# Kernel optimization log

Measured on AMD Instinct MI355X. Metric: run time of the kernel, lower is better.

Reference implementation:

```python
import jax, jax.numpy as jnp
import numpy as np

D = 2048        # hidden_size
F = 2048        # intermediate_size
E = 8           # num_local_experts
TOPK = 2        # num_experts_per_tok
ALPHA = 1.702   # gpt-oss swiglu alpha
LIMIT = 7.0     # gpt-oss clamp limit
AUX_COEF = 0.01


def setup_inputs() -> dict:
    key = jax.random.key(0)
    ks = jax.random.split(key, 7)
    s = 0.02
    return {
        "x": jax.random.normal(ks[0], (4, 1024, D), dtype=jnp.float32),
        "router_w": jax.random.normal(ks[1], (D, E), dtype=jnp.float32) * s,
        "router_b": jnp.zeros((E,), dtype=jnp.float32),
        "w_gate_up": jax.random.normal(ks[2], (E, D, 2 * F), dtype=jnp.float32) * s,
        "b_gate_up": jnp.zeros((E, 2 * F), dtype=jnp.float32),
        "w_down": jax.random.normal(ks[3], (E, F, D), dtype=jnp.float32) * s,
        "b_down": jnp.zeros((E, D), dtype=jnp.float32),
    }


def _moe(x, router_w, router_b, w_gate_up, b_gate_up, w_down, b_down):
    B, S, _ = x.shape
    xt = x.reshape(B * S, D)                                   # [T, D]
    T = xt.shape[0]

    # --- router ---
    logits = xt @ router_w + router_b                          # [T, E]
    full_probs = jax.nn.softmax(logits, axis=-1)               # [T, E]
    top_logits, top_idx = jax.lax.top_k(logits, TOPK)          # [T, k]
    routing_weights = jax.nn.softmax(top_logits, axis=-1)      # [T, k] (gpt-oss: softmax over top-k only)

    onehot = jax.nn.one_hot(top_idx, E, dtype=xt.dtype)        # [T, k, E]
    combine_w = jnp.einsum("tk,tke->te", routing_weights, onehot)  # [T, E]

    # --- experts (dense reference over all experts, masked combine) ---
    gu = jnp.einsum("td,edh->eth", xt, w_gate_up) + b_gate_up[:, None, :]  # [E, T, 2F]
    gate = gu[..., 0::2]                                       # interleaved gate
    up = gu[..., 1::2]                                         # interleaved up
    gate = jnp.minimum(gate, LIMIT)
    up = jnp.clip(up, -LIMIT, LIMIT)
    glu = gate * jax.nn.sigmoid(gate * ALPHA)
    act = (up + 1.0) * glu                                     # [E, T, F]
    expert_out = jnp.einsum("etf,efd->etd", act, w_down) + b_down[:, None, :]  # [E, T, D]

    out = jnp.einsum("etd,te->td", expert_out, combine_w).reshape(B, S, D)

    # --- routing stats / aux loss (Switch/Mixtral-style) ---
    dispatch_frac = jnp.mean(jnp.sum(onehot, axis=1), axis=0) / TOPK   # [E], sums to 1
    mean_probs = jnp.mean(full_probs, axis=0)                          # [E]
    expert_loads = dispatch_frac
    load_balancing_loss = AUX_COEF * E * jnp.sum(dispatch_frac * mean_probs)
    return out, expert_loads, load_balancing_loss


def reference(x, router_w, router_b, w_gate_up, b_gate_up, w_down, b_down):
    return _moe(x, router_w, router_b, w_gate_up, b_gate_up, w_down, b_down)
```

## Files before the change

kernel.cpp:

```cpp
#include <hip/hip_runtime.h>
#include <hip/hip_bf16.h>

#define TD 2048
#define TF 2048
#define NE 8
#define NT 4096
#define NTOPK 2

typedef __attribute__((ext_vector_type(4))) float f32x4;
typedef __attribute__((ext_vector_type(8))) short bf16x8;
typedef __attribute__((ext_vector_type(4))) short s16x4;

#define WS_XBF   ((size_t)0)
#define WS_ACT   ((size_t)16 << 20)
#define WS_WGU   ((size_t)48 << 20)
#define WS_WD    ((size_t)176 << 20)
#define WS_PROBS ((size_t)240 << 20)
#define WS_TOK   (WS_PROBS + (size_t)NT * NE * 4)
#define WS_WT    (WS_TOK + (size_t)NE * NT * 4)
#define WS_CNT   (WS_WT + (size_t)NE * NT * 4)
#define WS_OFF   (WS_CNT + 64)

__device__ __forceinline__ unsigned short f2bf(float f) {
  union { float f; unsigned u; } v; v.f = f;
  unsigned r = v.u + 0x7FFFu + ((v.u >> 16) & 1u);
  return (unsigned short)(r >> 16);
}

__device__ __forceinline__ void gload_lds16(const void* g, void* l) {
  __builtin_amdgcn_global_load_lds(
      (const __attribute__((address_space(1))) void*)g,
      (__attribute__((address_space(3))) void*)l, 16, 0, 0);
}

__global__ void k_cvt_x(const float* __restrict__ x, unsigned short* __restrict__ xbf) {
  int i = blockIdx.x * 256 + threadIdx.x;
  float4 v = ((const float4*)x)[i];
  s16x4 r;
  r[0] = (short)f2bf(v.x); r[1] = (short)f2bf(v.y);
  r[2] = (short)f2bf(v.z); r[3] = (short)f2bf(v.w);
  ((s16x4*)xbf)[i] = r;
}

__global__ void k_router(const float* __restrict__ x, const float* __restrict__ rw,
                         const float* __restrict__ rb, float* __restrict__ probs,
                         int* __restrict__ tok, float* __restrict__ wt,
                         int* __restrict__ counts) {
  const int t = blockIdx.x;
  const int l = threadIdx.x;
  const float* xr = x + (size_t)t * TD;
  float a0 = 0, a1 = 0, a2 = 0, a3 = 0, a4 = 0, a5 = 0, a6 = 0, a7 = 0;
#pragma unroll 4
  for (int j = 0; j < TD / 64; j++) {
    int d = j * 64 + l;
    float xv = xr[d];
    const float4* wp = (const float4*)(rw + (size_t)d * NE);
    float4 w0 = wp[0], w1 = wp[1];
    a0 += xv * w0.x; a1 += xv * w0.y; a2 += xv * w0.z; a3 += xv * w0.w;
    a4 += xv * w1.x; a5 += xv * w1.y; a6 += xv * w1.z; a7 += xv * w1.w;
  }
#pragma unroll
  for (int off = 32; off > 0; off >>= 1) {
    a0 += __shfl_xor(a0, off); a1 += __shfl_xor(a1, off);
    a2 += __shfl_xor(a2, off); a3 += __shfl_xor(a3, off);
    a4 += __shfl_xor(a4, off); a5 += __shfl_xor(a5, off);
    a6 += __shfl_xor(a6, off); a7 += __shfl_xor(a7, off);
  }
  if (l == 0) {
    float lg[NE] = { a0 + rb[0], a1 + rb[1], a2 + rb[2], a3 + rb[3],
                     a4 + rb[4], a5 + rb[5], a6 + rb[6], a7 + rb[7] };
    float mx = lg[0];
#pragma unroll
    for (int e = 1; e < NE; e++) mx = fmaxf(mx, lg[e]);
    float pe[NE]; float s = 0.f;
#pragma unroll
    for (int e = 0; e < NE; e++) { pe[e] = __expf(lg[e] - mx); s += pe[e]; }
    float inv = 1.f / s;
#pragma unroll
    for (int e = 0; e < NE; e++) probs[(size_t)t * NE + e] = pe[e] * inv;
    int i0 = 0; float b0 = lg[0];
#pragma unroll
    for (int e = 1; e < NE; e++) if (lg[e] > b0) { b0 = lg[e]; i0 = e; }
    int i1 = (i0 == 0) ? 1 : 0; float b1 = lg[i1];
#pragma unroll
    for (int e = 0; e < NE; e++)
      if (e != i0 && lg[e] > b1) { b1 = lg[e]; i1 = e; }
    float e1 = __expf(b1 - b0);
    float rs = 1.f / (1.f + e1);
    float w0v = rs;
    float w1v = e1 * rs;
    int p0 = atomicAdd(&counts[i0], 1);
    tok[i0 * NT + p0] = t; wt[i0 * NT + p0] = w0v;
    int p1 = atomicAdd(&counts[i1], 1);
    tok[i1 * NT + p1] = t; wt[i1 * NT + p1] = w1v;
  }
}

__global__ void k_finalize(const float* __restrict__ probs, const int* __restrict__ counts,
                           int* __restrict__ offsets, float* __restrict__ tail) {
  __shared__ float sh[4 * NE];
  int tid = threadIdx.x;
  float s[NE] = {0, 0, 0, 0, 0, 0, 0, 0};
  for (int t = tid; t < NT; t += 256) {
#pragma unroll
    for (int e = 0; e < NE; e++) s[e] += probs[(size_t)t * NE + e];
  }
#pragma unroll
  for (int off = 32; off > 0; off >>= 1) {
#pragma unroll
    for (int e = 0; e < NE; e++) s[e] += __shfl_xor(s[e], off);
  }
  if ((tid & 63) == 0) {
#pragma unroll
    for (int e = 0; e < NE; e++) sh[(tid >> 6) * NE + e] = s[e];
  }
  __syncthreads();
  if (tid == 0) {
    float loss = 0.f; int off = 0;
#pragma unroll
    for (int e = 0; e < NE; e++) {
      float mp = (sh[e] + sh[NE + e] + sh[2 * NE + e] + sh[3 * NE + e]) * (1.f / NT);
      int c = counts[e];
      offsets[e] = off; off += c;
      float df = (float)c / (float)(NT * NTOPK);
      tail[e] = df;
      loss += df * mp;
    }
    tail[NE] = 0.01f * (float)NE * loss;
  }
}

template <int REMAP>
__global__ void k_transpose(const float* __restrict__ W, unsigned short* __restrict__ Wt,
                            int R , int C ) {
  __shared__ unsigned short tile[64][72];
  const int e = blockIdx.z;
  const float* We = W + (size_t)e * R * C;
  unsigned short* Ot = Wt + (size_t)e * R * C;
  const int k0 = blockIdx.y * 64, c0 = blockIdx.x * 64;
  const int tid = threadIdx.x;
  {
    const int lr = tid >> 2, lq = tid & 3;
    const float* src = We + (size_t)(k0 + lr) * C + c0 + lq * 16;
#pragma unroll
    for (int q = 0; q < 4; q++) {
      float4 v = *(const float4*)(src + q * 4);
      int c = lq * 16 + q * 4;
      tile[lr][c + 0] = f2bf(v.x); tile[lr][c + 1] = f2bf(v.y);
      tile[lr][c + 2] = f2bf(v.z); tile[lr][c + 3] = f2bf(v.w);
    }
  }
  __syncthreads();
  {
    const int oc = tid >> 2, kq = tid & 3;
    const int n_src = c0 + oc;
    const int orow = REMAP ? ((n_src >> 1) + (n_src & 1) * TF) : n_src;
    unsigned short* dst = Ot + (size_t)orow * R + k0 + kq * 16;
#pragma unroll
    for (int g = 0; g < 4; g++) {
      s16x4 v;
#pragma unroll
      for (int i = 0; i < 4; i++) v[i] = (short)tile[kq * 16 + g * 4 + i][oc];
      *(s16x4*)(dst + g * 4) = v;
    }
  }
}

__global__ __launch_bounds__(256) void k_gemm1(
    const unsigned short* __restrict__ xbf, const int* __restrict__ tok,
    const int* __restrict__ counts, const int* __restrict__ offsets,
    const unsigned short* __restrict__ wgu, const float* __restrict__ bgu,
    unsigned short* __restrict__ act) {
  const int e = blockIdx.z;
  const int cnt = counts[e];
  const int m0 = blockIdx.y * 128;
  if (m0 >= cnt) return;
  const int n0 = blockIdx.x * 64;
  const int offe = offsets[e];
  const unsigned short* Bg = wgu + (size_t)e * (2 * TF) * TD;
  __shared__ unsigned short lA[128 * 32];
  __shared__ unsigned short lB[128 * 32];
  const int tid = threadIdx.x, wid = tid >> 6, lane = tid & 63;

  const unsigned short* srcA[2];
  const unsigned short* srcB[2];
#pragma unroll
  for (int j = 0; j < 2; j++) {
    int idx = j * 256 + tid, r = idx >> 2, q = idx & 3;
    int rr = min(m0 + r, cnt - 1);
    srcA[j] = xbf + (size_t)tok[e * NT + rr] * TD + q * 8;
    int srow = (r < 64) ? (n0 + r) : (TF + n0 + (r - 64));
    srcB[j] = Bg + (size_t)srow * TD + q * 8;
  }
  const int kc = (lane >> 4) * 8, cA = lane & 15;
  int aoff[2], boff[8];
#pragma unroll
  for (int mr = 0; mr < 2; mr++) aoff[mr] = (wid * 32 + mr * 16 + cA) * 32 + kc;
#pragma unroll
  for (int nf = 0; nf < 8; nf++) boff[nf] = (nf * 16 + cA) * 32 + kc;

  f32x4 acc[2][8] = {};

  for (int kt = 0; kt < TD / 32; kt++) {
    const int k0 = kt * 32;
    __syncthreads();
    gload_lds16(srcA[0] + k0, &lA[(size_t)tid * 8]);
    gload_lds16(srcA[1] + k0, &lA[(size_t)(256 + tid) * 8]);
    gload_lds16(srcB[0] + k0, &lB[(size_t)tid * 8]);
    gload_lds16(srcB[1] + k0, &lB[(size_t)(256 + tid) * 8]);
    __syncthreads();
    bf16x8 af0 = *(const bf16x8*)&lA[aoff[0]];
    bf16x8 af1 = *(const bf16x8*)&lA[aoff[1]];
#pragma unroll
    for (int nf = 0; nf < 8; nf++) {
      bf16x8 bfr = *(const bf16x8*)&lB[boff[nf]];
      acc[0][nf] = __builtin_amdgcn_mfma_f32_16x16x32_bf16(af0, bfr, acc[0][nf], 0, 0, 0);
      acc[1][nf] = __builtin_amdgcn_mfma_f32_16x16x32_bf16(af1, bfr, acc[1][nf], 0, 0, 0);
    }
  }

  const float* be = bgu + (size_t)e * 2 * TF;
#pragma unroll
  for (int nf = 0; nf < 4; nf++) {
    int col = n0 + nf * 16 + cA;
    float bgate = be[2 * col], bup = be[2 * col + 1];
#pragma unroll
    for (int mr = 0; mr < 2; mr++) {
#pragma unroll
      for (int r = 0; r < 4; r++) {
        int row = wid * 32 + mr * 16 + (lane >> 4) * 4 + r;
        if (m0 + row < cnt) {
          float g = acc[mr][nf][r] + bgate;
          float u = acc[mr][nf + 4][r] + bup;
          g = fminf(g, 7.0f);
          u = fminf(fmaxf(u, -7.0f), 7.0f);
          float glu = g * (1.0f / (1.0f + __expf(-1.702f * g)));
          float a = (u + 1.0f) * glu;
          act[(size_t)(offe + m0 + row) * TF + col] = f2bf(a);
        }
      }
    }
  }
}

__global__ __launch_bounds__(256) void k_gemm2(
    const unsigned short* __restrict__ act, const int* __restrict__ tok,
    const float* __restrict__ wt, const int* __restrict__ counts,
    const int* __restrict__ offsets, const unsigned short* __restrict__ wd,
    const float* __restrict__ bd, float* __restrict__ out) {
  const int e = blockIdx.z;
  const int cnt = counts[e];
  const int m0 = blockIdx.y * 128;
  if (m0 >= cnt) return;
  const int d0 = blockIdx.x * 128;
  const int offe = offsets[e];
  const unsigned short* Bd = wd + (size_t)e * TD * TF;
  __shared__ unsigned short lA[128 * 32];
  __shared__ unsigned short lB[128 * 32];
  const int tid = threadIdx.x, wid = tid >> 6, lane = tid & 63;

  const unsigned short* srcA[2];
  const unsigned short* srcB[2];
#pragma unroll
  for (int j = 0; j < 2; j++) {
    int idx = j * 256 + tid, r = idx >> 2, q = idx & 3;
    int rr = min(m0 + r, cnt - 1);
    srcA[j] = act + (size_t)(offe + rr) * TF + q * 8;
    srcB[j] = Bd + (size_t)(d0 + r) * TF + q * 8;
  }
  const int kc = (lane >> 4) * 8, cA = lane & 15;
  int aoff[2], boff[8];
#pragma unroll
  for (int mr = 0; mr < 2; mr++) aoff[mr] = (wid * 32 + mr * 16 + cA) * 32 + kc;
#pragma unroll
  for (int nf = 0; nf < 8; nf++) boff[nf] = (nf * 16 + cA) * 32 + kc;

  f32x4 acc[2][8] = {};

  for (int kt = 0; kt < TF / 32; kt++) {
    const int k0 = kt * 32;
    __syncthreads();
    gload_lds16(srcA[0] + k0, &lA[(size_t)tid * 8]);
    gload_lds16(srcA[1] + k0, &lA[(size_t)(256 + tid) * 8]);
    gload_lds16(srcB[0] + k0, &lB[(size_t)tid * 8]);
    gload_lds16(srcB[1] + k0, &lB[(size_t)(256 + tid) * 8]);
    __syncthreads();
    bf16x8 af0 = *(const bf16x8*)&lA[aoff[0]];
    bf16x8 af1 = *(const bf16x8*)&lA[aoff[1]];
#pragma unroll
    for (int nf = 0; nf < 8; nf++) {
      bf16x8 bfr = *(const bf16x8*)&lB[boff[nf]];
      acc[0][nf] = __builtin_amdgcn_mfma_f32_16x16x32_bf16(af0, bfr, acc[0][nf], 0, 0, 0);
      acc[1][nf] = __builtin_amdgcn_mfma_f32_16x16x32_bf16(af1, bfr, acc[1][nf], 0, 0, 0);
    }
  }

  const float* bde = bd + (size_t)e * TD;
#pragma unroll
  for (int nf = 0; nf < 8; nf++) {
    int col = d0 + nf * 16 + cA;
    float bc = bde[col];
#pragma unroll
    for (int mr = 0; mr < 2; mr++) {
#pragma unroll
      for (int r = 0; r < 4; r++) {
        int row = wid * 32 + mr * 16 + (lane >> 4) * 4 + r;
        int rowe = m0 + row;
        if (rowe < cnt) {
          float v = acc[mr][nf][r] + bc;
          int tk = tok[e * NT + rowe];
          float w = wt[e * NT + rowe];
          atomicAdd(&out[(size_t)tk * TD + col], w * v);
        }
      }
    }
  }
}

extern "C" void kernel_launch(void* const* d_in, const int* in_sizes, int n_in,
                              void* d_out, int out_size, void* d_ws, size_t ws_size,
                              hipStream_t stream) {
  const float* x   = (const float*)d_in[0];
  const float* rw  = (const float*)d_in[1];
  const float* rb  = (const float*)d_in[2];
  const float* wgu = (const float*)d_in[3];
  const float* bgu = (const float*)d_in[4];
  const float* wdn = (const float*)d_in[5];
  const float* bdn = (const float*)d_in[6];
  float* out = (float*)d_out;
  char* ws = (char*)d_ws;

  unsigned short* xbf  = (unsigned short*)(ws + WS_XBF);
  unsigned short* act  = (unsigned short*)(ws + WS_ACT);
  unsigned short* wgut = (unsigned short*)(ws + WS_WGU);
  unsigned short* wdt  = (unsigned short*)(ws + WS_WD);
  float* probs = (float*)(ws + WS_PROBS);
  int*   tokl  = (int*)(ws + WS_TOK);
  float* wtl   = (float*)(ws + WS_WT);
  int*   cnts  = (int*)(ws + WS_CNT);
  int*   offs  = (int*)(ws + WS_OFF);

  hipMemsetAsync(out, 0, (size_t)NT * TD * sizeof(float), stream);
  hipMemsetAsync(cnts, 0, NE * sizeof(int), stream);

  k_cvt_x<<<(NT * TD) / 1024, 256, 0, stream>>>(x, xbf);
  k_router<<<NT, 64, 0, stream>>>(x, rw, rb, probs, tokl, wtl, cnts);
  k_finalize<<<1, 256, 0, stream>>>(probs, cnts, offs, out + (size_t)NT * TD);
  k_transpose<1><<<dim3(4096 / 64, 2048 / 64, NE), 256, 0, stream>>>(wgu, wgut, TD, 2 * TF);
  k_transpose<0><<<dim3(2048 / 64, 2048 / 64, NE), 256, 0, stream>>>(wdn, wdt, TF, TD);
  k_gemm1<<<dim3(TF / 64, NT / 128, NE), 256, 0, stream>>>(xbf, tokl, cnts, offs, wgut, bgu, act);
  k_gemm2<<<dim3(TD / 128, NT / 128, NE), 256, 0, stream>>>(act, tokl, wtl, cnts, offs, wdt, bdn, out);
}
```

Measured before the change: 1.016 ms.

## Replace atomic scatter with gather combine, retile GEMM warps, widen transpose tiles

The router now records each token's two (expert, slot) pairs so the down-projection can write weighted rows into a contiguous per-slot buffer. A separate combine kernel then gathers and sums them, which removes the float atomics and the memset of the output. Both GEMMs switch from a 1x4 warp layout (2x8 fragments per warp) to a 2x2 layout (4x4 fragments) to improve fragment reuse from LDS. Grid axes are swapped so consecutive blocks share weight columns. The weight transpose uses larger 256-row tiles with XOR-swizzled LDS and 16-byte stores. In exchange it adds a 64 MB intermediate buffer write and read plus one extra launch.

```diff
diff --git a/kernel.cpp b/kernel.cpp
--- a/kernel.cpp
+++ b/kernel.cpp
@@ -14,11 +14,13 @@
 #define WS_XBF   ((size_t)0)
 #define WS_ACT   ((size_t)16 << 20)
 #define WS_WGU   ((size_t)48 << 20)
+#define WS_EO    ((size_t)48 << 20)
 #define WS_WD    ((size_t)176 << 20)
 #define WS_PROBS ((size_t)240 << 20)
 #define WS_TOK   (WS_PROBS + (size_t)NT * NE * 4)
 #define WS_WT    (WS_TOK + (size_t)NE * NT * 4)
-#define WS_CNT   (WS_WT + (size_t)NE * NT * 4)
+#define WS_INV   (WS_WT + (size_t)NE * NT * 4)
+#define WS_CNT   (WS_INV + (size_t)NT * 16)
 #define WS_OFF   (WS_CNT + 64)
 
 __device__ __forceinline__ unsigned short f2bf(float f) {
@@ -45,7 +47,7 @@
 __global__ void k_router(const float* __restrict__ x, const float* __restrict__ rw,
                          const float* __restrict__ rb, float* __restrict__ probs,
                          int* __restrict__ tok, float* __restrict__ wt,
-                         int* __restrict__ counts) {
+                         int4* __restrict__ inv, int* __restrict__ counts) {
   const int t = blockIdx.x;
   const int l = threadIdx.x;
   const float* xr = x + (size_t)t * TD;
@@ -75,9 +77,9 @@
     float pe[NE]; float s = 0.f;
 #pragma unroll
     for (int e = 0; e < NE; e++) { pe[e] = __expf(lg[e] - mx); s += pe[e]; }
-    float inv = 1.f / s;
-#pragma unroll
-    for (int e = 0; e < NE; e++) probs[(size_t)t * NE + e] = pe[e] * inv;
+    float inv_s = 1.f / s;
+#pragma unroll
+    for (int e = 0; e < NE; e++) probs[(size_t)t * NE + e] = pe[e] * inv_s;
     int i0 = 0; float b0 = lg[0];
 #pragma unroll
     for (int e = 1; e < NE; e++) if (lg[e] > b0) { b0 = lg[e]; i0 = e; }
@@ -93,6 +95,7 @@
     tok[i0 * NT + p0] = t; wt[i0 * NT + p0] = w0v;
     int p1 = atomicAdd(&counts[i1], 1);
     tok[i1 * NT + p1] = t; wt[i1 * NT + p1] = w1v;
+    inv[t] = make_int4(i0, p0, i1, p1);
   }
 }
 
@@ -131,37 +134,42 @@
 }
 
 template <int REMAP>
-__global__ void k_transpose(const float* __restrict__ W, unsigned short* __restrict__ Wt,
-                            int R , int C ) {
-  __shared__ unsigned short tile[64][72];
+__global__ __launch_bounds__(256) void k_transpose(
+    const float* __restrict__ W, unsigned short* __restrict__ Wt, int R, int C) {
+  __shared__ unsigned short lds[256 * 64];
   const int e = blockIdx.z;
   const float* We = W + (size_t)e * R * C;
   unsigned short* Ot = Wt + (size_t)e * R * C;
-  const int k0 = blockIdx.y * 64, c0 = blockIdx.x * 64;
+  const int k0 = blockIdx.y * 256, c0 = blockIdx.x * 64;
   const int tid = threadIdx.x;
   {
-    const int lr = tid >> 2, lq = tid & 3;
-    const float* src = We + (size_t)(k0 + lr) * C + c0 + lq * 16;
-#pragma unroll
-    for (int q = 0; q < 4; q++) {
-      float4 v = *(const float4*)(src + q * 4);
-      int c = lq * 16 + q * 4;
-      tile[lr][c + 0] = f2bf(v.x); tile[lr][c + 1] = f2bf(v.y);
-      tile[lr][c + 2] = f2bf(v.z); tile[lr][c + 3] = f2bf(v.w);
+    const int rsub = tid >> 4;
+    const int cq = tid & 15;
+#pragma unroll
+    for (int p = 0; p < 16; p++) {
+      int row = p * 16 + rsub;
+      float4 v = *(const float4*)(We + (size_t)(k0 + row) * C + c0 + cq * 4);
+      s16x4 b;
+      b[0] = f2bf(v.x); b[1] = f2bf(v.y); b[2] = f2bf(v.z); b[3] = f2bf(v.w);
+      *(s16x4*)&lds[row * 64 + ((cq ^ (row & 15)) << 2)] = b;
     }
   }
   __syncthreads();
   {
-    const int oc = tid >> 2, kq = tid & 3;
-    const int n_src = c0 + oc;
+    const int c = tid & 63, seg = tid >> 6;
+    const int n_src = c0 + c;
     const int orow = REMAP ? ((n_src >> 1) + (n_src & 1) * TF) : n_src;
-    unsigned short* dst = Ot + (size_t)orow * R + k0 + kq * 16;
-#pragma unroll
-    for (int g = 0; g < 4; g++) {
-      s16x4 v;
-#pragma unroll
-      for (int i = 0; i < 4; i++) v[i] = (short)tile[kq * 16 + g * 4 + i][oc];
-      *(s16x4*)(dst + g * 4) = v;
+    unsigned short* dst = Ot + (size_t)orow * R + k0 + seg * 64;
+    const int ccq = c >> 2, cr = c & 3;
+#pragma unroll
+    for (int g = 0; g < 8; g++) {
+      bf16x8 val;
+#pragma unroll
+      for (int ii = 0; ii < 8; ii++) {
+        int k = seg * 64 + g * 8 + ii;
+        val[ii] = (short)lds[k * 64 + (((ccq ^ (k & 15)) << 2) | cr)];
+      }
+      *(bf16x8*)(dst + g * 8) = val;
     }
   }
 }
@@ -173,14 +181,15 @@
     unsigned short* __restrict__ act) {
   const int e = blockIdx.z;
   const int cnt = counts[e];
-  const int m0 = blockIdx.y * 128;
+  const int m0 = blockIdx.x * 128;
   if (m0 >= cnt) return;
-  const int n0 = blockIdx.x * 64;
+  const int n0 = blockIdx.y * 64;
   const int offe = offsets[e];
   const unsigned short* Bg = wgu + (size_t)e * (2 * TF) * TD;
   __shared__ unsigned short lA[128 * 32];
   __shared__ unsigned short lB[128 * 32];
   const int tid = threadIdx.x, wid = tid >> 6, lane = tid & 63;
+  const int wr = wid >> 1, wc = wid & 1;
 
   const unsigned short* srcA[2];
   const unsigned short* srcB[2];
@@ -192,14 +201,17 @@
     int srow = (r < 64) ? (n0 + r) : (TF + n0 + (r - 64));
     srcB[j] = Bg + (size_t)srow * TD + q * 8;
   }
-  const int kc = (lane >> 4) * 8, cA = lane & 15;
-  int aoff[2], boff[8];
-#pragma unroll
-  for (int mr = 0; mr < 2; mr++) aoff[mr] = (wid * 32 + mr * 16 + cA) * 32 + kc;
-#pragma unroll
-  for (int nf = 0; nf < 8; nf++) boff[nf] = (nf * 16 + cA) * 32 + kc;
-
-  f32x4 acc[2][8] = {};
+  const int cA = lane & 15, q = lane >> 4, kc = q * 8;
+  int aoff[4], boff[4];
+#pragma unroll
+  for (int m = 0; m < 4; m++) aoff[m] = (wr * 64 + m * 16 + cA) * 32 + kc;
+#pragma unroll
+  for (int n = 0; n < 4; n++) {
+    int brow = (n < 2) ? (wc * 32 + n * 16) : (64 + wc * 32 + (n - 2) * 16);
+    boff[n] = (brow + cA) * 32 + kc;
+  }
+
+  f32x4 acc[4][4] = {};
 
   for (int kt = 0; kt < TD / 32; kt++) {
     const int k0 = kt * 32;
@@ -209,29 +221,31 @@
     gload_lds16(srcB[0] + k0, &lB[(size_t)tid * 8]);
     gload_lds16(srcB[1] + k0, &lB[(size_t)(256 + tid) * 8]);
     __syncthreads();
-    bf16x8 af0 = *(const bf16x8*)&lA[aoff[0]];
-    bf16x8 af1 = *(const bf16x8*)&lA[aoff[1]];
-#pragma unroll
-    for (int nf = 0; nf < 8; nf++) {
-      bf16x8 bfr = *(const bf16x8*)&lB[boff[nf]];
-      acc[0][nf] = __builtin_amdgcn_mfma_f32_16x16x32_bf16(af0, bfr, acc[0][nf], 0, 0, 0);
-      acc[1][nf] = __builtin_amdgcn_mfma_f32_16x16x32_bf16(af1, bfr, acc[1][nf], 0, 0, 0);
+    bf16x8 af[4];
+#pragma unroll
+    for (int m = 0; m < 4; m++) af[m] = *(const bf16x8*)&lA[aoff[m]];
+#pragma unroll
+    for (int n = 0; n < 4; n++) {
+      bf16x8 bfr = *(const bf16x8*)&lB[boff[n]];
+#pragma unroll
+      for (int m = 0; m < 4; m++)
+        acc[m][n] = __builtin_amdgcn_mfma_f32_16x16x32_bf16(af[m], bfr, acc[m][n], 0, 0, 0);
     }
   }
 
   const float* be = bgu + (size_t)e * 2 * TF;
 #pragma unroll
-  for (int nf = 0; nf < 4; nf++) {
-    int col = n0 + nf * 16 + cA;
-    float bgate = be[2 * col], bup = be[2 * col + 1];
-#pragma unroll
-    for (int mr = 0; mr < 2; mr++) {
+  for (int n = 0; n < 2; n++) {
+    int col = n0 + wc * 32 + n * 16 + cA;
+    float bg = be[2 * col], bu = be[2 * col + 1];
+#pragma unroll
+    for (int m = 0; m < 4; m++) {
 #pragma unroll
       for (int r = 0; r < 4; r++) {
-        int row = wid * 32 + mr * 16 + (lane >> 4) * 4 + r;
+        int row = wr * 64 + m * 16 + q * 4 + r;
         if (m0 + row < cnt) {
-          float g = acc[mr][nf][r] + bgate;
-          float u = acc[mr][nf + 4][r] + bup;
+          float g = acc[m][n][r] + bg;
+          float u = acc[m][n + 2][r] + bu;
           g = fminf(g, 7.0f);
           u = fminf(fmaxf(u, -7.0f), 7.0f);
           float glu = g * (1.0f / (1.0f + __expf(-1.702f * g)));
@@ -244,20 +258,21 @@
 }
 
 __global__ __launch_bounds__(256) void k_gemm2(
-    const unsigned short* __restrict__ act, const int* __restrict__ tok,
-    const float* __restrict__ wt, const int* __restrict__ counts,
-    const int* __restrict__ offsets, const unsigned short* __restrict__ wd,
-    const float* __restrict__ bd, float* __restrict__ out) {
+    const unsigned short* __restrict__ act, const float* __restrict__ wt,
+    const int* __restrict__ counts, const int* __restrict__ offsets,
+    const unsigned short* __restrict__ wd, const float* __restrict__ bd,
+    float* __restrict__ eo) {
   const int e = blockIdx.z;
   const int cnt = counts[e];
-  const int m0 = blockIdx.y * 128;
+  const int m0 = blockIdx.x * 128;
   if (m0 >= cnt) return;
-  const int d0 = blockIdx.x * 128;
+  const int d0 = blockIdx.y * 128;
   const int offe = offsets[e];
   const unsigned short* Bd = wd + (size_t)e * TD * TF;
   __shared__ unsigned short lA[128 * 32];
   __shared__ unsigned short lB[128 * 32];
   const int tid = threadIdx.x, wid = tid >> 6, lane = tid & 63;
+  const int wr = wid >> 1, wc = wid & 1;
 
   const unsigned short* srcA[2];
   const unsigned short* srcB[2];
@@ -268,14 +283,14 @@
     srcA[j] = act + (size_t)(offe + rr) * TF + q * 8;
     srcB[j] = Bd + (size_t)(d0 + r) * TF + q * 8;
   }
-  const int kc = (lane >> 4) * 8, cA = lane & 15;
-  int aoff[2], boff[8];
-#pragma unroll
-  for (int mr = 0; mr < 2; mr++) aoff[mr] = (wid * 32 + mr * 16 + cA) * 32 + kc;
-#pragma unroll
-  for (int nf = 0; nf < 8; nf++) boff[nf] = (nf * 16 + cA) * 32 + kc;
-
-  f32x4 acc[2][8] = {};
+  const int cA = lane & 15, q = lane >> 4, kc = q * 8;
+  int aoff[4], boff[4];
+#pragma unroll
+  for (int m = 0; m < 4; m++) aoff[m] = (wr * 64 + m * 16 + cA) * 32 + kc;
+#pragma unroll
+  for (int n = 0; n < 4; n++) boff[n] = (wc * 64 + n * 16 + cA) * 32 + kc;
+
+  f32x4 acc[4][4] = {};
 
   for (int kt = 0; kt < TF / 32; kt++) {
     const int k0 = kt * 32;
@@ -285,36 +300,49 @@
     gload_lds16(srcB[0] + k0, &lB[(size_t)tid * 8]);
     gload_lds16(srcB[1] + k0, &lB[(size_t)(256 + tid) * 8]);
     __syncthreads();
-    bf16x8 af0 = *(const bf16x8*)&lA[aoff[0]];
-    bf16x8 af1 = *(const bf16x8*)&lA[aoff[1]];
-#pragma unroll
-    for (int nf = 0; nf < 8; nf++) {
-      bf16x8 bfr = *(const bf16x8*)&lB[boff[nf]];
-      acc[0][nf] = __builtin_amdgcn_mfma_f32_16x16x32_bf16(af0, bfr, acc[0][nf], 0, 0, 0);
-      acc[1][nf] = __builtin_amdgcn_mfma_f32_16x16x32_bf16(af1, bfr, acc[1][nf], 0, 0, 0);
+    bf16x8 af[4];
+#pragma unroll
+    for (int m = 0; m < 4; m++) af[m] = *(const bf16x8*)&lA[aoff[m]];
+#pragma unroll
+    for (int n = 0; n < 4; n++) {
+      bf16x8 bfr = *(const bf16x8*)&lB[boff[n]];
+#pragma unroll
+      for (int m = 0; m < 4; m++)
+        acc[m][n] = __builtin_amdgcn_mfma_f32_16x16x32_bf16(af[m], bfr, acc[m][n], 0, 0, 0);
     }
   }
 
   const float* bde = bd + (size_t)e * TD;
 #pragma unroll
-  for (int nf = 0; nf < 8; nf++) {
-    int col = d0 + nf * 16 + cA;
+  for (int n = 0; n < 4; n++) {
+    int col = d0 + wc * 64 + n * 16 + cA;
     float bc = bde[col];
 #pragma unroll
-    for (int mr = 0; mr < 2; mr++) {
+    for (int m = 0; m < 4; m++) {
 #pragma unroll
       for (int r = 0; r < 4; r++) {
-        int row = wid * 32 + mr * 16 + (lane >> 4) * 4 + r;
+        int row = wr * 64 + m * 16 + q * 4 + r;
         int rowe = m0 + row;
         if (rowe < cnt) {
-          float v = acc[mr][nf][r] + bc;
-          int tk = tok[e * NT + rowe];
           float w = wt[e * NT + rowe];
-          atomicAdd(&out[(size_t)tk * TD + col], w * v);
+          eo[(size_t)(offe + rowe) * TD + col] = w * (acc[m][n][r] + bc);
         }
       }
     }
   }
+}
+
+__global__ void k_combine(const float* __restrict__ eo, const int4* __restrict__ inv,
+                          const int* __restrict__ offs, float* __restrict__ out) {
+  int i = blockIdx.x * 256 + threadIdx.x;
+  int t = i >> 9;
+  int c = i & 511;
+  int4 v = inv[t];
+  int s0 = offs[v.x] + v.y, s1 = offs[v.z] + v.w;
+  float4 a = ((const float4*)eo)[(size_t)s0 * 512 + c];
+  float4 b = ((const float4*)eo)[(size_t)s1 * 512 + c];
+  float4 r; r.x = a.x + b.x; r.y = a.y + b.y; r.z = a.z + b.z; r.w = a.w + b.w;
+  ((float4*)out)[i] = r;
 }
 
 extern "C" void kernel_launch(void* const* d_in, const int* in_sizes, int n_in,
@@ -334,20 +362,22 @@
   unsigned short* act  = (unsigned short*)(ws + WS_ACT);
   unsigned short* wgut = (unsigned short*)(ws + WS_WGU);
   unsigned short* wdt  = (unsigned short*)(ws + WS_WD);
+  float* eo    = (float*)(ws + WS_EO);
   float* probs = (float*)(ws + WS_PROBS);
   int*   tokl  = (int*)(ws + WS_TOK);
   float* wtl   = (float*)(ws + WS_WT);
+  int4*  invm  = (int4*)(ws + WS_INV);
   int*   cnts  = (int*)(ws + WS_CNT);
   int*   offs  = (int*)(ws + WS_OFF);
 
-  hipMemsetAsync(out, 0, (size_t)NT * TD * sizeof(float), stream);
   hipMemsetAsync(cnts, 0, NE * sizeof(int), stream);
 
   k_cvt_x<<<(NT * TD) / 1024, 256, 0, stream>>>(x, xbf);
-  k_router<<<NT, 64, 0, stream>>>(x, rw, rb, probs, tokl, wtl, cnts);
+  k_router<<<NT, 64, 0, stream>>>(x, rw, rb, probs, tokl, wtl, invm, cnts);
   k_finalize<<<1, 256, 0, stream>>>(probs, cnts, offs, out + (size_t)NT * TD);
-  k_transpose<1><<<dim3(4096 / 64, 2048 / 64, NE), 256, 0, stream>>>(wgu, wgut, TD, 2 * TF);
-  k_transpose<0><<<dim3(2048 / 64, 2048 / 64, NE), 256, 0, stream>>>(wdn, wdt, TF, TD);
-  k_gemm1<<<dim3(TF / 64, NT / 128, NE), 256, 0, stream>>>(xbf, tokl, cnts, offs, wgut, bgu, act);
-  k_gemm2<<<dim3(TD / 128, NT / 128, NE), 256, 0, stream>>>(act, tokl, wtl, cnts, offs, wdt, bdn, out);
-}
+  k_transpose<1><<<dim3(4096 / 64, 2048 / 256, NE), 256, 0, stream>>>(wgu, wgut, TD, 2 * TF);
+  k_transpose<0><<<dim3(2048 / 64, 2048 / 256, NE), 256, 0, stream>>>(wdn, wdt, TF, TD);
+  k_gemm1<<<dim3(NT / 128, TF / 64, NE), 256, 0, stream>>>(xbf, tokl, cnts, offs, wgut, bgu, act);
+  k_gemm2<<<dim3(NT / 128, TD / 128, NE), 256, 0, stream>>>(act, wtl, cnts, offs, wdt, bdn, eo);
+  k_combine<<<(NT * TD) / 1024, 256, 0, stream>>>(eo, invm, offs, out);
+}
```

After: 1.677 ms. +65.1%, slower.
